# Optimization experiments

Hardware: AMD Instinct MI355X
Metric: run time of the kernel (lower is better)

The kernel has to match this reference:

```python
import jax, jax.numpy as jnp
import numpy as np

BIOSYNTHETIC_FAMILIES = {'glutamate': ['E','Q','P','R','K'], 'aspartate': ['D','N','T','I','M','K'], 'serine': ['S','G','C'], 'pyruvate': ['A','V','L'], 'aromatic': ['F','Y','W'], 'histidine': ['H']}
CODON_TABLE = {'UUU':'F','UUC':'F','UUA':'L','UUG':'L','CUU':'L','CUC':'L','CUA':'L','CUG':'L','AUU':'I','AUC':'I','AUA':'I','AUG':'M','GUU':'V','GUC':'V','GUA':'V','GUG':'V','UCU':'S','UCC':'S','UCA':'S','UCG':'S','CCU':'P','CCC':'P','CCA':'P','CCG':'P','ACU':'T','ACC':'T','ACA':'T','ACG':'T','GCU':'A','GCC':'A','GCA':'A','GCG':'A','UAU':'Y','UAC':'Y','UAA':'*','UAG':'*','CAU':'H','CAC':'H','CAA':'Q','CAG':'Q','AAU':'N','AAC':'N','AAA':'K','AAG':'K','GAU':'D','GAC':'D','GAA':'E','GAG':'E','UGU':'C','UGC':'C','UGA':'*','UGG':'W','CGU':'R','CGC':'R','CGA':'R','CGG':'R','AGU':'S','AGC':'S','AGA':'R','AGG':'R','GGU':'G','GGC':'G','GGA':'G','GGG':'G'}

def _build_family_matrix():
    aa2fam = {aa: f for f, aas in BIOSYNTHETIC_FAMILIES.items() for aa in aas}
    codons = list(CODON_TABLE.keys())
    fam = [aa2fam.get(CODON_TABLE[c]) for c in codons]  # None for stop codons
    M = np.zeros((64, 64), dtype=np.float32)
    for i in range(64):
        for j in range(64):
            if fam[i] is not None and fam[j] is not None and fam[i] == fam[j]:
                M[i, j] = 1.0
    return jnp.asarray(M)

FAMILY_MATRIX = _build_family_matrix()  # (64, 64) constant lookup table

def setup_inputs() -> dict:
    key = jax.random.key(0)
    k1, k2 = jax.random.split(key)
    codon_embeddings = jax.random.normal(k1, (16, 512, 16), dtype=jnp.float32)
    codon_indices = jax.random.randint(k2, (16, 512), 0, 64, dtype=jnp.int64 if jax.config.jax_enable_x64 else jnp.int32)
    return {"codon_embeddings": codon_embeddings, "codon_indices": codon_indices}

def reference(codon_embeddings, codon_indices):
    b, s, d = codon_embeddings.shape
    emb = codon_embeddings.reshape(-1, d)            # (n, d)
    idx = codon_indices.reshape(-1)                  # (n,)
    # Euclidean pairwise distances (torch.cdist, p=2)
    sq = jnp.sum(emb * emb, axis=-1)                 # (n,)
    d2 = sq[:, None] + sq[None, :] - 2.0 * (emb @ emb.T)
    d2 = jnp.maximum(d2, 0.0)
    mask = d2 > 0.0
    dist = jnp.where(mask, jnp.sqrt(jnp.where(mask, d2, 1.0)), 0.0)  # (n, n)
    # Same-family mask via 64x64 lookup gather
    same = FAMILY_MATRIX[idx[:, None], idx[None, :]]  # (n, n)
    eps = 1e-10
    same_sum = jnp.sum(same)
    total = jnp.asarray(dist.shape[0] * dist.shape[1], dist.dtype)
    same_d = jnp.sum(dist * same) / (same_sum + eps)
    diff_d = (jnp.sum(dist) - jnp.sum(dist * same)) / ((total - same_sum) + eps)
    loss = same_d - 0.5 * diff_d + 1.0
    return jax.nn.relu(loss)
```

## Files before the change

kernel.cpp:

```cpp
#include <hip/hip_runtime.h>
#include <math.h>

#define N_ROWS 8192
#define D 16
#define TILE 128
#define NT 64
#define NPAIR 1056

#define OFF_PT   0
#define OFF_PS   8192

typedef short  bf16x8 __attribute__((ext_vector_type(8)));
typedef float  f32x4  __attribute__((ext_vector_type(4)));

#define BF_ONE ((unsigned short)0x3F80)

__device__ __constant__ signed char FAM_LUT[64] = {
  4,4,3,3, 3,3,3,3,
  1,1,1,1, 3,3,3,3,
  2,2,2,2, 0,0,0,0,
  1,1,1,1, 3,3,3,3,
  4,4,-1,-1, 5,5,0,0,
  1,1,1,1, 1,1,0,0,
  2,2,-1,4, 0,0,0,0,
  2,2,0,0, 2,2,2,2
};

__device__ __forceinline__ unsigned short f2bf(float f) {
  unsigned u = __float_as_uint(f);
  u += 0x7fffu + ((u >> 16) & 1u);
  return (unsigned short)(u >> 16);
}
__device__ __forceinline__ float bf2f(unsigned short s) {
  return __uint_as_float((unsigned)s << 16);
}
__device__ __forceinline__ float sqrt_abs(float x) {
  float r;
  asm("v_sqrt_f32 %0, abs(%1)" : "=v"(r) : "v"(x));
  return r;
}
__device__ __forceinline__ int S_of(int m) {
  return (m & 1) ? (((m + 1) * (m + 1)) >> 2) : ((m * (m + 2)) >> 2);
}

__global__ __launch_bounds__(512, 4) void pair_kernel(
    const float* __restrict__ emb, const int* __restrict__ idx,
    float* __restrict__ pt, float* __restrict__ ps) {
  const int b = blockIdx.x;
  const int cc = NPAIR - b;
  int m = (int)(2.0f * sqrtf((float)cc));
  if (m > NT) m = NT;
  if (m < 1) m = 1;
  while (S_of(m) < cc) ++m;
  while (m > 1 && S_of(m - 1) >= cc) --m;
  const int it  = NT - m;
  const int p   = b - (NPAIR - S_of(m));
  const int jt0 = it + 2 * p;
  const int jt1 = jt0 + 1;
  const bool v1 = (jt1 < NT);

  __shared__ __align__(16) unsigned short LB1[8192];
  __shared__ __align__(16) unsigned short LFB[2048];
  __shared__ __align__(16) unsigned short LFA[1024];
  __shared__ __align__(16) unsigned short LZ[8];
  __shared__ float SQIF[TILE];
  __shared__ float rT[8], rS[8];

  const int t  = threadIdx.x;
  const int w  = t >> 6;
  const int l  = t & 63;
  const int lr = l & 15;
  const int g  = l >> 4;

  if (t < 256) {
    const int  jd    = t >> 7;
    const int  rl    = t & 127;
    const int  jtile = jd ? jt1 : jt0;
    const bool valid = (jtile < NT);
    const int  row   = min(jtile, NT - 1) * TILE + rl;
    const float4* s4 = (const float4*)(emb + (size_t)row * D);
    float4 a0 = s4[0], a1 = s4[1], a2 = s4[2], a3 = s4[3];
    float v[16];
    v[0]=a0.x; v[1]=a0.y; v[2]=a0.z; v[3]=a0.w;
    v[4]=a1.x; v[5]=a1.y; v[6]=a1.z; v[7]=a1.w;
    v[8]=a2.x; v[9]=a2.y; v[10]=a2.z; v[11]=a2.w;
    v[12]=a3.x; v[13]=a3.y; v[14]=a3.z; v[15]=a3.w;
    unsigned short bh[16];
#pragma unroll
    for (int k = 0; k < 16; ++k) bh[k] = valid ? f2bf(v[k]) : (unsigned short)0;
    float ss = bf2f(bh[0]) * bf2f(bh[0]);
#pragma unroll
    for (int k = 1; k < 16; ++k) { const float rv = bf2f(bh[k]); ss = fmaf(rv, rv, ss); }
    const unsigned short sqh = f2bf(ss);
    const unsigned short sql = f2bf(ss - bf2f(sqh));
    unsigned short c2[8] = {sqh, sql, BF_ONE, BF_ONE, 0, 0, 0, 0};
    if (!valid) { c2[0] = 0; c2[1] = 0; c2[2] = 0; c2[3] = 0; }
    unsigned short cz[8] = {0, 0, 0, 0, 0, 0, 0, 0};
    unsigned short* d1 = LB1 + t * 32;
    *(bf16x8*)(d1 + 0)  = *(bf16x8*)&bh[0];
    *(bf16x8*)(d1 + 8)  = *(bf16x8*)&bh[8];
    *(bf16x8*)(d1 + 16) = *(bf16x8*)c2;
    *(bf16x8*)(d1 + 24) = *(bf16x8*)cz;
    const int f = valid ? FAM_LUT[idx[row] & 63] : -9;
    unsigned short oh[8];
#pragma unroll
    for (int k = 0; k < 8; ++k) oh[k] = (f == k) ? BF_ONE : (unsigned short)0;
    *(bf16x8*)(LFB + t * 8) = *(bf16x8*)oh;
  } else if (t < 384) {
    const int local = t - 256;
    const int row = it * TILE + local;
    const float4* s4 = (const float4*)(emb + (size_t)row * D);
    float4 a0 = s4[0], a1 = s4[1], a2 = s4[2], a3 = s4[3];
    float v[16];
    v[0]=a0.x; v[1]=a0.y; v[2]=a0.z; v[3]=a0.w;
    v[4]=a1.x; v[5]=a1.y; v[6]=a1.z; v[7]=a1.w;
    v[8]=a2.x; v[9]=a2.y; v[10]=a2.z; v[11]=a2.w;
    v[12]=a3.x; v[13]=a3.y; v[14]=a3.z; v[15]=a3.w;
    float ss = 0.0f;
#pragma unroll
    for (int k = 0; k < 16; ++k) { const float rv = bf2f(f2bf(v[k])); ss = fmaf(rv, rv, ss); }
    SQIF[local] = ss;
    const int f = FAM_LUT[idx[row] & 63];
    unsigned short oh[8];
#pragma unroll
    for (int k = 0; k < 8; ++k) oh[k] = (f == k) ? BF_ONE : (unsigned short)0;
    *(bf16x8*)(LFA + local * 8) = *(bf16x8*)oh;
  } else if (t == 384) {
    bf16x8 z = {0,0,0,0,0,0,0,0};
    *(bf16x8*)LZ = z;
  }

  const int arow = it * TILE + w * 16 + lr;
  const float4* a4 = (const float4*)(emb + (size_t)arow * D + (g & 1) * 8);
  float4 c0 = a4[0], c1 = a4[1];
  float va[8];
  va[0]=c0.x; va[1]=c0.y; va[2]=c0.z; va[3]=c0.w;
  va[4]=c1.x; va[5]=c1.y; va[6]=c1.z; va[7]=c1.w;
  unsigned short f8[8];
#pragma unroll
  for (int k = 0; k < 8; ++k) f8[k] = f2bf(-2.0f * bf2f(f2bf(va[k])));

  __syncthreads();

  if (g >= 2) {
#pragma unroll
    for (int k = 0; k < 8; ++k) f8[k] = 0;
    if (g == 2) {
      const float sq = SQIF[w * 16 + lr];
      const unsigned short sqh = f2bf(sq);
      f8[0] = BF_ONE; f8[1] = BF_ONE;
      f8[2] = sqh;    f8[3] = f2bf(sq - bf2f(sqh));
    }
  }
  const bf16x8 afrag = *(bf16x8*)f8;
  bf16x8 afrag3;
  if (g == 0) afrag3 = *(const bf16x8*)(LFA + (w * 16 + lr) * 8);
  else        { bf16x8 z = {0,0,0,0,0,0,0,0}; afrag3 = z; }

  const unsigned short* p3 = (g == 0) ? (LFB + lr * 8) : LZ;
  const int step3 = (g == 0) ? 128 : 0;
  const int boff  = lr * 32 + g * 8;
  const f32x4 zf = {0.0f, 0.0f, 0.0f, 0.0f};
  float tT0 = 0.0f, tS0 = 0.0f, tT1 = 0.0f, tS1 = 0.0f;
#pragma unroll
  for (int mj = 0; mj < 16; ++mj) {
    const bf16x8 b1f = *(const bf16x8*)(LB1 + (mj * 16) * 32 + boff);
    const bf16x8 m3  = *(const bf16x8*)(p3 + mj * step3);
    const f32x4 acc = __builtin_amdgcn_mfma_f32_16x16x32_bf16(afrag,  b1f, zf, 0, 0, 0);
    const f32x4 msk = __builtin_amdgcn_mfma_f32_16x16x32_bf16(afrag3, m3,  zf, 0, 0, 0);
#pragma unroll
    for (int r = 0; r < 4; ++r) {
      const float dist = sqrt_abs(acc[r]);
      if (mj < 8) { tT0 += dist; tS0 = fmaf(msk[r], dist, tS0); }
      else        { tT1 += dist; tS1 = fmaf(msk[r], dist, tS1); }
    }
  }

  const float w0 = (jt0 == it) ? 1.0f : 2.0f;
  const float w1 = v1 ? 2.0f : 0.0f;
  float accT = fmaf(w0, tT0, w1 * tT1);
  float accS = fmaf(w0, tS0, w1 * tS1);
#pragma unroll
  for (int off = 32; off > 0; off >>= 1) {
    accT += __shfl_down(accT, off);
    accS += __shfl_down(accS, off);
  }
  if (l == 0) { rT[w] = accT; rS[w] = accS; }
  __syncthreads();
  if (t == 0) {
    float sT = 0.0f, sS = 0.0f;
#pragma unroll
    for (int k = 0; k < 8; ++k) { sT += rT[k]; sS += rS[k]; }
    pt[b] = sT;
    ps[b] = sS;
  }
}

__global__ __launch_bounds__(1024) void final_kernel(
    const float* __restrict__ pt, const float* __restrict__ ps,
    const int* __restrict__ idx, float* __restrict__ out) {
  const int t = threadIdx.x, w = t >> 6, l = t & 63;
  __shared__ float  HW[16][8];
  __shared__ double rTd[16], rSd[16];

  const int4* p4 = (const int4*)idx;
  const int4 va = p4[t], vb = p4[t + 1024];
  int vals[8] = {va.x, va.y, va.z, va.w, vb.x, vb.y, vb.z, vb.w};
  float myCnt = 0.0f;
#pragma unroll
  for (int rr = 0; rr < 8; ++rr) {
    const int f = FAM_LUT[vals[rr] & 63];
#pragma unroll
    for (int fam = 0; fam < 6; ++fam) {
      const unsigned long long mk = __ballot(f == fam);
      if (l == fam) myCnt += (float)__popcll(mk);
    }
  }
  if (l < 8) HW[w][l] = (l < 6) ? myCnt : 0.0f;

  double sT = 0.0, sS = 0.0;
  for (int k = t; k < NPAIR; k += 1024) { sT += (double)pt[k]; sS += (double)ps[k]; }
#pragma unroll
  for (int off = 32; off > 0; off >>= 1) {
    sT += __shfl_down(sT, off);
    sS += __shfl_down(sS, off);
  }
  if (l == 0) { rTd[w] = sT; rSd[w] = sS; }
  __syncthreads();
  if (t == 0) {
    double tot = 0.0, sam = 0.0;
#pragma unroll
    for (int k = 0; k < 16; ++k) { tot += rTd[k]; sam += rSd[k]; }
    double same_sum = 0.0;
    for (int f = 0; f < 6; ++f) {
      double c = 0.0;
      for (int k = 0; k < 16; ++k) c += (double)HW[k][f];
      same_sum += c * c;
    }
    const double total  = (double)N_ROWS * (double)N_ROWS;
    const double same_d = sam / (same_sum + 1e-10);
    const double diff_d = (tot - sam) / (total - same_sum + 1e-10);
    double loss = same_d - 0.5 * diff_d + 1.0;
    out[0] = (float)(loss > 0.0 ? loss : 0.0);
  }
}

extern "C" void kernel_launch(void* const* d_in, const int* in_sizes, int n_in,
                              void* d_out, int out_size, void* d_ws, size_t ws_size,
                              hipStream_t stream) {
  const float* emb = (const float*)d_in[0];
  const int*   idx = (const int*)d_in[1];
  char* ws = (char*)d_ws;
  float* pt = (float*)(ws + OFF_PT);
  float* ps = (float*)(ws + OFF_PS);

  pair_kernel<<<dim3(NPAIR), dim3(512), 0, stream>>>(emb, idx, pt, ps);
  final_kernel<<<dim3(1), dim3(1024), 0, stream>>>(pt, ps, idx, (float*)d_out);
}
```

Baseline: 21.93 us.

## Process four column tiles per block instead of two to halve grid size

Each block now covers one row tile against four consecutive column tiles of the upper triangle (quads) rather than two. The grid drops from 1056 to 544 blocks, and each block stages 512 B-rows into LDS and runs 32 MFMA steps. The aim is to amortise the per-block A-tile load, setup and reduction over more work. In exchange LDS use per block roughly doubles, which may reduce occupancy, and more tiles at the triangle edge are padding past NT.

```diff
diff --git a/kernel.cpp b/kernel.cpp
--- a/kernel.cpp
+++ b/kernel.cpp
@@ -5,10 +5,10 @@
 #define D 16
 #define TILE 128
 #define NT 64
-#define NPAIR 1056
+#define NQUAD 544
 
 #define OFF_PT   0
-#define OFF_PS   8192
+#define OFF_PS   4096
 
 typedef short  bf16x8 __attribute__((ext_vector_type(8)));
 typedef float  f32x4  __attribute__((ext_vector_type(4)));
@@ -39,28 +39,27 @@
   asm("v_sqrt_f32 %0, abs(%1)" : "=v"(r) : "v"(x));
   return r;
 }
-__device__ __forceinline__ int S_of(int m) {
-  return (m & 1) ? (((m + 1) * (m + 1)) >> 2) : ((m * (m + 2)) >> 2);
+__device__ __forceinline__ int S4_of(int m) {
+  const int q = m >> 2, r = m & 3;
+  return 2 * q * (q + 1) + r * (q + 1);
 }
 
 __global__ __launch_bounds__(512, 4) void pair_kernel(
     const float* __restrict__ emb, const int* __restrict__ idx,
     float* __restrict__ pt, float* __restrict__ ps) {
   const int b = blockIdx.x;
-  const int cc = NPAIR - b;
-  int m = (int)(2.0f * sqrtf((float)cc));
+  const int cc = NQUAD - b;
+  int m = (int)sqrtf(8.0f * (float)cc);
   if (m > NT) m = NT;
   if (m < 1) m = 1;
-  while (S_of(m) < cc) ++m;
-  while (m > 1 && S_of(m - 1) >= cc) --m;
+  while (S4_of(m) < cc) ++m;
+  while (m > 1 && S4_of(m - 1) >= cc) --m;
   const int it  = NT - m;
-  const int p   = b - (NPAIR - S_of(m));
-  const int jt0 = it + 2 * p;
-  const int jt1 = jt0 + 1;
-  const bool v1 = (jt1 < NT);
-
-  __shared__ __align__(16) unsigned short LB1[8192];
-  __shared__ __align__(16) unsigned short LFB[2048];
+  const int p   = b - (NQUAD - S4_of(m));
+  const int jtb = it + 4 * p;
+
+  __shared__ __align__(16) unsigned short LB1[16384];
+  __shared__ __align__(16) unsigned short LFB[4096];
   __shared__ __align__(16) unsigned short LFA[1024];
   __shared__ __align__(16) unsigned short LZ[8];
   __shared__ float SQIF[TILE];
@@ -72,10 +71,10 @@
   const int lr = l & 15;
   const int g  = l >> 4;
 
-  if (t < 256) {
+  {
     const int  jd    = t >> 7;
     const int  rl    = t & 127;
-    const int  jtile = jd ? jt1 : jt0;
+    const int  jtile = jtb + jd;
     const bool valid = (jtile < NT);
     const int  row   = min(jtile, NT - 1) * TILE + rl;
     const float4* s4 = (const float4*)(emb + (size_t)row * D);
@@ -106,9 +105,10 @@
 #pragma unroll
     for (int k = 0; k < 8; ++k) oh[k] = (f == k) ? BF_ONE : (unsigned short)0;
     *(bf16x8*)(LFB + t * 8) = *(bf16x8*)oh;
-  } else if (t < 384) {
-    const int local = t - 256;
-    const int row = it * TILE + local;
+  }
+
+  if (t < 128) {
+    const int row = it * TILE + t;
     const float4* s4 = (const float4*)(emb + (size_t)row * D);
     float4 a0 = s4[0], a1 = s4[1], a2 = s4[2], a3 = s4[3];
     float v[16];
@@ -119,13 +119,13 @@
     float ss = 0.0f;
 #pragma unroll
     for (int k = 0; k < 16; ++k) { const float rv = bf2f(f2bf(v[k])); ss = fmaf(rv, rv, ss); }
-    SQIF[local] = ss;
+    SQIF[t] = ss;
     const int f = FAM_LUT[idx[row] & 63];
     unsigned short oh[8];
 #pragma unroll
     for (int k = 0; k < 8; ++k) oh[k] = (f == k) ? BF_ONE : (unsigned short)0;
-    *(bf16x8*)(LFA + local * 8) = *(bf16x8*)oh;
-  } else if (t == 384) {
+    *(bf16x8*)(LFA + t * 8) = *(bf16x8*)oh;
+  } else if (t == 128) {
     bf16x8 z = {0,0,0,0,0,0,0,0};
     *(bf16x8*)LZ = z;
   }
@@ -161,25 +161,27 @@
   const int step3 = (g == 0) ? 128 : 0;
   const int boff  = lr * 32 + g * 8;
   const f32x4 zf = {0.0f, 0.0f, 0.0f, 0.0f};
-  float tT0 = 0.0f, tS0 = 0.0f, tT1 = 0.0f, tS1 = 0.0f;
-#pragma unroll
-  for (int mj = 0; mj < 16; ++mj) {
-    const bf16x8 b1f = *(const bf16x8*)(LB1 + (mj * 16) * 32 + boff);
+  float tT[4] = {0.f, 0.f, 0.f, 0.f}, tS[4] = {0.f, 0.f, 0.f, 0.f};
+#pragma unroll
+  for (int mj = 0; mj < 32; ++mj) {
+    const bf16x8 b1f = *(const bf16x8*)(LB1 + mj * 512 + boff);
     const bf16x8 m3  = *(const bf16x8*)(p3 + mj * step3);
     const f32x4 acc = __builtin_amdgcn_mfma_f32_16x16x32_bf16(afrag,  b1f, zf, 0, 0, 0);
     const f32x4 msk = __builtin_amdgcn_mfma_f32_16x16x32_bf16(afrag3, m3,  zf, 0, 0, 0);
 #pragma unroll
     for (int r = 0; r < 4; ++r) {
       const float dist = sqrt_abs(acc[r]);
-      if (mj < 8) { tT0 += dist; tS0 = fmaf(msk[r], dist, tS0); }
-      else        { tT1 += dist; tS1 = fmaf(msk[r], dist, tS1); }
-    }
-  }
-
-  const float w0 = (jt0 == it) ? 1.0f : 2.0f;
-  const float w1 = v1 ? 2.0f : 0.0f;
-  float accT = fmaf(w0, tT0, w1 * tT1);
-  float accS = fmaf(w0, tS0, w1 * tS1);
+      tT[mj >> 3] += dist;
+      tS[mj >> 3] = fmaf(msk[r], dist, tS[mj >> 3]);
+    }
+  }
+
+  const float w0 = (p == 0) ? 1.0f : 2.0f;
+  const float w1 = (jtb + 1 < NT) ? 2.0f : 0.0f;
+  const float w2 = (jtb + 2 < NT) ? 2.0f : 0.0f;
+  const float w3 = (jtb + 3 < NT) ? 2.0f : 0.0f;
+  float accT = fmaf(w0, tT[0], fmaf(w1, tT[1], fmaf(w2, tT[2], w3 * tT[3])));
+  float accS = fmaf(w0, tS[0], fmaf(w1, tS[1], fmaf(w2, tS[2], w3 * tS[3])));
 #pragma unroll
   for (int off = 32; off > 0; off >>= 1) {
     accT += __shfl_down(accT, off);
@@ -219,7 +221,7 @@
   if (l < 8) HW[w][l] = (l < 6) ? myCnt : 0.0f;
 
   double sT = 0.0, sS = 0.0;
-  for (int k = t; k < NPAIR; k += 1024) { sT += (double)pt[k]; sS += (double)ps[k]; }
+  if (t < NQUAD) { sT = (double)pt[t]; sS = (double)ps[t]; }
 #pragma unroll
   for (int off = 32; off > 0; off >>= 1) {
     sT += __shfl_down(sT, off);
@@ -254,6 +256,6 @@
   float* pt = (float*)(ws + OFF_PT);
   float* ps = (float*)(ws + OFF_PS);
 
-  pair_kernel<<<dim3(NPAIR), dim3(512), 0, stream>>>(emb, idx, pt, ps);
+  pair_kernel<<<dim3(NQUAD), dim3(512), 0, stream>>>(emb, idx, pt, ps);
   final_kernel<<<dim3(1), dim3(1024), 0, stream>>>(pt, ps, idx, (float*)d_out);
 }
```

Measured after the change: 22.60 us. +3.0%, slower.

## Fuse final reduction into pair kernel via last-block atomic pattern

Applied to the files above, without the earlier changes.

Removes the separate single-block final kernel. Each block converts its partial sums to fixed-point 64-bit integers and adds them atomically, then increments a done counter, and the last block to finish computes the family counts and the loss. A memset of the workspace is added before the launch. This saves a kernel launch and its dependency gap, at the cost of an extra memset operation, atomics on two addresses, and fixed-point rounding in the accumulated sums.

```diff
diff --git a/kernel.cpp b/kernel.cpp
--- a/kernel.cpp
+++ b/kernel.cpp
@@ -6,9 +6,9 @@
 #define TILE 128
 #define NT 64
 #define NPAIR 1056
-
-#define OFF_PT   0
-#define OFF_PS   8192
+#define SCALE_F 16777216.0f
+#define INV_SCALE 5.9604644775390625e-08
+
 
 typedef short  bf16x8 __attribute__((ext_vector_type(8)));
 typedef float  f32x4  __attribute__((ext_vector_type(4)));
@@ -45,7 +45,8 @@
 
 __global__ __launch_bounds__(512, 4) void pair_kernel(
     const float* __restrict__ emb, const int* __restrict__ idx,
-    float* __restrict__ pt, float* __restrict__ ps) {
+    unsigned int* __restrict__ done, unsigned long long* __restrict__ sums,
+    float* __restrict__ out) {
   const int b = blockIdx.x;
   const int cc = NPAIR - b;
   int m = (int)(2.0f * sqrtf((float)cc));
@@ -65,6 +66,8 @@
   __shared__ __align__(16) unsigned short LZ[8];
   __shared__ float SQIF[TILE];
   __shared__ float rT[8], rS[8];
+  __shared__ float HW[8][8];
+  __shared__ int amLast;
 
   const int t  = threadIdx.x;
   const int w  = t >> 6;
@@ -164,7 +167,7 @@
   float tT0 = 0.0f, tS0 = 0.0f, tT1 = 0.0f, tS1 = 0.0f;
 #pragma unroll
   for (int mj = 0; mj < 16; ++mj) {
-    const bf16x8 b1f = *(const bf16x8*)(LB1 + (mj * 16) * 32 + boff);
+    const bf16x8 b1f = *(const bf16x8*)(LB1 + mj * 512 + boff);
     const bf16x8 m3  = *(const bf16x8*)(p3 + mj * step3);
     const f32x4 acc = __builtin_amdgcn_mfma_f32_16x16x32_bf16(afrag,  b1f, zf, 0, 0, 0);
     const f32x4 msk = __builtin_amdgcn_mfma_f32_16x16x32_bf16(afrag3, m3,  zf, 0, 0, 0);
@@ -191,50 +194,43 @@
     float sT = 0.0f, sS = 0.0f;
 #pragma unroll
     for (int k = 0; k < 8; ++k) { sT += rT[k]; sS += rS[k]; }
-    pt[b] = sT;
-    ps[b] = sS;
-  }
-}
-
-__global__ __launch_bounds__(1024) void final_kernel(
-    const float* __restrict__ pt, const float* __restrict__ ps,
-    const int* __restrict__ idx, float* __restrict__ out) {
-  const int t = threadIdx.x, w = t >> 6, l = t & 63;
-  __shared__ float  HW[16][8];
-  __shared__ double rTd[16], rSd[16];
-
-  const int4* p4 = (const int4*)idx;
-  const int4 va = p4[t], vb = p4[t + 1024];
-  int vals[8] = {va.x, va.y, va.z, va.w, vb.x, vb.y, vb.z, vb.w};
+    const unsigned long long iT = (unsigned long long)(sT * SCALE_F + 0.5f);
+    const unsigned long long iS = (unsigned long long)(sS * SCALE_F + 0.5f);
+    atomicAdd(&sums[0], iT);
+    atomicAdd(&sums[1], iS);
+    __threadfence();
+    amLast = (atomicAdd(done, 1u) == NPAIR - 1);
+  }
+  __syncthreads();
+  if (!amLast) return;
+
   float myCnt = 0.0f;
-#pragma unroll
-  for (int rr = 0; rr < 8; ++rr) {
-    const int f = FAM_LUT[vals[rr] & 63];
-#pragma unroll
-    for (int fam = 0; fam < 6; ++fam) {
-      const unsigned long long mk = __ballot(f == fam);
-      if (l == fam) myCnt += (float)__popcll(mk);
+  const int4* p4i = (const int4*)idx;
+#pragma unroll
+  for (int rr = 0; rr < 4; ++rr) {
+    const int4 vv = p4i[rr * 512 + t];
+    const int v4[4] = {vv.x, vv.y, vv.z, vv.w};
+#pragma unroll
+    for (int e = 0; e < 4; ++e) {
+      const int f = FAM_LUT[v4[e] & 63];
+#pragma unroll
+      for (int fam = 0; fam < 6; ++fam) {
+        const unsigned long long mk = __ballot(f == fam);
+        if (l == fam) myCnt += (float)__popcll(mk);
+      }
     }
   }
   if (l < 8) HW[w][l] = (l < 6) ? myCnt : 0.0f;
-
-  double sT = 0.0, sS = 0.0;
-  for (int k = t; k < NPAIR; k += 1024) { sT += (double)pt[k]; sS += (double)ps[k]; }
-#pragma unroll
-  for (int off = 32; off > 0; off >>= 1) {
-    sT += __shfl_down(sT, off);
-    sS += __shfl_down(sS, off);
-  }
-  if (l == 0) { rTd[w] = sT; rSd[w] = sS; }
   __syncthreads();
   if (t == 0) {
-    double tot = 0.0, sam = 0.0;
-#pragma unroll
-    for (int k = 0; k < 16; ++k) { tot += rTd[k]; sam += rSd[k]; }
+    const unsigned long long vT = atomicAdd(&sums[0], 0ull);
+    const unsigned long long vS = atomicAdd(&sums[1], 0ull);
+    const double tot = (double)vT * INV_SCALE;
+    const double sam = (double)vS * INV_SCALE;
     double same_sum = 0.0;
     for (int f = 0; f < 6; ++f) {
       double c = 0.0;
-      for (int k = 0; k < 16; ++k) c += (double)HW[k][f];
+      for (int k = 0; k < 8; ++k) c += (double)HW[k][f];
       same_sum += c * c;
     }
     const double total  = (double)N_ROWS * (double)N_ROWS;
@@ -251,9 +247,10 @@
   const float* emb = (const float*)d_in[0];
   const int*   idx = (const int*)d_in[1];
   char* ws = (char*)d_ws;
-  float* pt = (float*)(ws + OFF_PT);
-  float* ps = (float*)(ws + OFF_PS);
-
-  pair_kernel<<<dim3(NPAIR), dim3(512), 0, stream>>>(emb, idx, pt, ps);
-  final_kernel<<<dim3(1), dim3(1024), 0, stream>>>(pt, ps, idx, (float*)d_out);
-}
+  unsigned int*       done = (unsigned int*)(ws);
+  unsigned long long* sums = (unsigned long long*)(ws + 8);
+
+  hipMemsetAsync(ws, 0, 64, stream);
+  pair_kernel<<<dim3(NPAIR), dim3(512), 0, stream>>>(emb, idx, done, sums,
+                                                     (float*)d_out);
+}
```

New measurement: 59.32 us. +170.5%, slower.
